# Kernel tuning notes

Measured on AMD Instinct MI355X. Metric: run time of the kernel, lower is better.

Reference implementation:

```python
import jax, jax.numpy as jnp
import numpy as np

N, D = 8192, 4096  # D must be a power of 2 for FWHT


def fwht(x):
    """Unnormalized Fast Walsh-Hadamard Transform along the last axis (len = 2^k)."""
    orig_shape = x.shape
    d = orig_shape[-1]
    x = x.reshape(-1, d)
    h = 1
    while h < d:
        x = x.reshape(-1, d // (2 * h), 2, h)
        a = x[..., 0, :]
        b = x[..., 1, :]
        x = jnp.stack([a + b, a - b], axis=-2)
        h *= 2
    return x.reshape(orig_shape)


def setup_inputs() -> dict:
    key = jax.random.key(0)
    k = jax.random.split(key, 6)
    return {
        "x": jax.random.normal(k[0], (N, D), dtype=jnp.float32),
        "s1": jax.random.normal(k[1], (D,), dtype=jnp.float32),
        "s2": jax.random.normal(k[2], (D,), dtype=jnp.float32),
        "g_mu": jax.random.normal(k[3], (D,), dtype=jnp.float32),
        "g_rho": jax.random.normal(k[4], (D,), dtype=jnpp.float32) if False else jax.random.normal(k[4], (D,), dtype=jnp.float32),
        "epsilon": jax.random.normal(k[5], (D,), dtype=jnp.float32),
    }


def reference(x, s1, s2, g_mu, g_rho, epsilon):
    # W(u) = diag(s1) H diag(u) H diag(s2); forward (sample=True):
    #   b = x @ W(g_mu).T + x @ W(softplus(g_rho) * epsilon).T
    # Per-row (H symmetric): x @ W(u).T = s1 * fwht(u * fwht(s2 * x)).
    t = fwht(x * s2)                                  # [N, D], shared between both terms
    g_noise = jax.nn.softplus(g_rho) * epsilon        # g_sigma_sqrt @ epsilon
    b = s1 * fwht(t * g_mu) + s1 * fwht(t * g_noise)  # [N, D]
    return b
```

## Files before the change

### kernel.cpp

```cpp
#include <hip/hip_runtime.h>
#include <math.h>

#define D 4096

__device__ __forceinline__ void fwht64(float* v) {
#pragma unroll
    for (int h = 1; h < 64; h <<= 1) {
#pragma unroll
        for (int i = 0; i < 64; i += 2 * h) {
#pragma unroll
            for (int j = i; j < i + h; ++j) {
                const float a = v[j];
                const float b = v[j + h];
                v[j]     = a + b;
                v[j + h] = a - b;
            }
        }
    }
}

__global__ void whvi_prep(const float* __restrict__ g_mu,
                          const float* __restrict__ g_rho,
                          const float* __restrict__ eps,
                          float* __restrict__ gq) {
    const int i = blockIdx.x * 64 + threadIdx.x;
    const int l = i >> 6, k = i & 63;
    const int e = (l & 3) | (k << 2) | ((l >> 2) << 8);
    const float r  = g_rho[e];
    const float sp = (r > 20.f) ? r : log1pf(expf(r));
    gq[i] = g_mu[e] + sp * eps[e];
}

__global__ void __launch_bounds__(64) whvi_main(
    const float* __restrict__ x,  const float* __restrict__ s1,
    const float* __restrict__ s2, const float* __restrict__ gq,
    const float* __restrict__ g_mu, const float* __restrict__ g_rho,
    const float* __restrict__ eps, float* __restrict__ out) {
    __shared__ alignas(16) float lds[D];
    const int l = threadIdx.x;
    const long long row = blockIdx.x;
    const float* xr = x + row * (long long)D;
    float v[64];

#pragma unroll
    for (int q = 0; q < 16; ++q) {
        const int base = (l << 2) + (q << 8);
        const float4 xv = *reinterpret_cast<const float4*>(xr + base);
        const float4 sv = *reinterpret_cast<const float4*>(s2 + base);
        v[4 * q + 0] = xv.x * sv.x;
        v[4 * q + 1] = xv.y * sv.y;
        v[4 * q + 2] = xv.z * sv.z;
        v[4 * q + 3] = xv.w * sv.w;
    }

    fwht64(v);

#pragma unroll
    for (int q = 0; q < 16; ++q) {
        const int addr = ((l ^ (q & 7)) << 2) + (q << 8);
        *reinterpret_cast<float4*>(&lds[addr]) =
            make_float4(v[4 * q], v[4 * q + 1], v[4 * q + 2], v[4 * q + 3]);
    }
    __syncthreads();
    {
        const int xb = (l & 3) | ((l >> 2) << 8);
        const int mk = (l >> 2) & 7;
#pragma unroll
        for (int k = 0; k < 64; ++k)
            v[k] = lds[xb + ((k ^ mk) << 2)];
    }

    fwht64(v);

    if (gq) {
#pragma unroll
        for (int m = 0; m < 16; ++m) {
            const float4 gv = *reinterpret_cast<const float4*>(gq + l * 64 + 4 * m);
            v[4 * m + 0] *= gv.x;
            v[4 * m + 1] *= gv.y;
            v[4 * m + 2] *= gv.z;
            v[4 * m + 3] *= gv.w;
        }
    } else {
#pragma unroll
        for (int k = 0; k < 64; ++k) {
            const int e = (l & 3) | (k << 2) | ((l >> 2) << 8);
            const float r  = g_rho[e];
            const float sp = (r > 20.f) ? r : log1pf(expf(r));
            v[k] *= g_mu[e] + sp * eps[e];
        }
    }

    fwht64(v);

    __syncthreads();
    {
        const int xb = (l & 3) | ((l >> 2) << 8);
        const int mk = (l >> 2) & 7;
#pragma unroll
        for (int k = 0; k < 64; ++k)
            lds[xb + ((k ^ mk) << 2)] = v[k];
    }
    __syncthreads();
#pragma unroll
    for (int q = 0; q < 16; ++q) {
        const int addr = ((l ^ (q & 7)) << 2) + (q << 8);
        const float4 t = *reinterpret_cast<const float4*>(&lds[addr]);
        v[4 * q + 0] = t.x;
        v[4 * q + 1] = t.y;
        v[4 * q + 2] = t.z;
        v[4 * q + 3] = t.w;
    }

    fwht64(v);

    float* outr = out + row * (long long)D;
#pragma unroll
    for (int q = 0; q < 16; ++q) {
        const int base = (l << 2) + (q << 8);
        const float4 sv = *reinterpret_cast<const float4*>(s1 + base);
        float4 o;
        o.x = v[4 * q + 0] * sv.x;
        o.y = v[4 * q + 1] * sv.y;
        o.z = v[4 * q + 2] * sv.z;
        o.w = v[4 * q + 3] * sv.w;
        *reinterpret_cast<float4*>(outr + base) = o;
    }
}

extern "C" void kernel_launch(void* const* d_in, const int* in_sizes, int n_in,
                              void* d_out, int out_size, void* d_ws, size_t ws_size,
                              hipStream_t stream) {
    const float* x     = (const float*)d_in[0];
    const float* s1    = (const float*)d_in[1];
    const float* s2    = (const float*)d_in[2];
    const float* g_mu  = (const float*)d_in[3];
    const float* g_rho = (const float*)d_in[4];
    const float* eps   = (const float*)d_in[5];
    float* out = (float*)d_out;
    const int rows = in_sizes[0] / D;

    float* gq = nullptr;
    if (ws_size >= (size_t)D * sizeof(float)) {
        gq = (float*)d_ws;
        whvi_prep<<<D / 64, 64, 0, stream>>>(g_mu, g_rho, eps, gq);
    }
    whvi_main<<<rows, 64, 0, stream>>>(x, s1, s2, gq, g_mu, g_rho, eps, out);
}
```

Before: 249.9 us.

## Halve LDS footprint by doing each transpose in two half-passes

The shared-memory transpose between FWHT stages now uses a 2048-float buffer instead of 4096. Each transpose runs as two sequential half-exchanges: each half-wave writes its half, reads its half, then swaps roles, with extra barriers in between. A min-blocks hint of 4 is added to the launch bounds. The goal is to fit more single-wave blocks per CU to hide global-memory latency, at the cost of extra barriers and LDS round trips.

```diff
diff --git a/kernel.cpp b/kernel.cpp
--- a/kernel.cpp
+++ b/kernel.cpp
@@ -31,16 +31,20 @@
     gq[i] = g_mu[e] + sp * eps[e];
 }
 
-__global__ void __launch_bounds__(64) whvi_main(
+__global__ void __launch_bounds__(64, 4) whvi_main(
     const float* __restrict__ x,  const float* __restrict__ s1,
     const float* __restrict__ s2, const float* __restrict__ gq,
     const float* __restrict__ g_mu, const float* __restrict__ g_rho,
     const float* __restrict__ eps, float* __restrict__ out) {
-    __shared__ alignas(16) float lds[D];
-    const int l = threadIdx.x;
+    __shared__ alignas(16) float lds[2048];
+    const int l  = threadIdx.x;
+    const int hi = l >> 5;
     const long long row = blockIdx.x;
     const float* xr = x + row * (long long)D;
     float v[64];
+
+#define WA(q) ((((l ^ ((q) & 7)) & 31) << 2) + ((q) << 7))
+#define RB(k) (xb + ((((k) ^ mk) & 31) << 2))
 
 #pragma unroll
     for (int q = 0; q < 16; ++q) {
@@ -55,19 +59,47 @@
 
     fwht64(v);
 
-#pragma unroll
-    for (int q = 0; q < 16; ++q) {
-        const int addr = ((l ^ (q & 7)) << 2) + (q << 8);
-        *reinterpret_cast<float4*>(&lds[addr]) =
-            make_float4(v[4 * q], v[4 * q + 1], v[4 * q + 2], v[4 * q + 3]);
-    }
-    __syncthreads();
-    {
-        const int xb = (l & 3) | ((l >> 2) << 8);
-        const int mk = (l >> 2) & 7;
-#pragma unroll
-        for (int k = 0; k < 64; ++k)
-            v[k] = lds[xb + ((k ^ mk) << 2)];
+    const int mk = (l >> 2) & 7;
+    const int xb = (l & 3) + ((l >> 2) << 7);
+
+    if (hi == 0) {
+#pragma unroll
+        for (int q = 0; q < 8; ++q)
+            *reinterpret_cast<float4*>(&lds[WA(q)]) =
+                make_float4(v[4*q], v[4*q+1], v[4*q+2], v[4*q+3]);
+    } else {
+#pragma unroll
+        for (int q = 8; q < 16; ++q)
+            *reinterpret_cast<float4*>(&lds[WA(q)]) =
+                make_float4(v[4*q], v[4*q+1], v[4*q+2], v[4*q+3]);
+    }
+    __syncthreads();
+    if (hi == 0) {
+#pragma unroll
+        for (int k = 0; k < 32; ++k) v[k] = lds[RB(k)];
+    } else {
+#pragma unroll
+        for (int k = 32; k < 64; ++k) v[k] = lds[RB(k)];
+    }
+    __syncthreads();
+    if (hi == 0) {
+#pragma unroll
+        for (int q = 8; q < 16; ++q)
+            *reinterpret_cast<float4*>(&lds[WA(q)]) =
+                make_float4(v[4*q], v[4*q+1], v[4*q+2], v[4*q+3]);
+    } else {
+#pragma unroll
+        for (int q = 0; q < 8; ++q)
+            *reinterpret_cast<float4*>(&lds[WA(q)]) =
+                make_float4(v[4*q], v[4*q+1], v[4*q+2], v[4*q+3]);
+    }
+    __syncthreads();
+    if (hi == 0) {
+#pragma unroll
+        for (int k = 32; k < 64; ++k) v[k] = lds[RB(k)];
+    } else {
+#pragma unroll
+        for (int k = 0; k < 32; ++k) v[k] = lds[RB(k)];
     }
 
     fwht64(v);
@@ -94,22 +126,48 @@
     fwht64(v);
 
     __syncthreads();
-    {
-        const int xb = (l & 3) | ((l >> 2) << 8);
-        const int mk = (l >> 2) & 7;
-#pragma unroll
-        for (int k = 0; k < 64; ++k)
-            lds[xb + ((k ^ mk) << 2)] = v[k];
-    }
-    __syncthreads();
-#pragma unroll
-    for (int q = 0; q < 16; ++q) {
-        const int addr = ((l ^ (q & 7)) << 2) + (q << 8);
-        const float4 t = *reinterpret_cast<const float4*>(&lds[addr]);
-        v[4 * q + 0] = t.x;
-        v[4 * q + 1] = t.y;
-        v[4 * q + 2] = t.z;
-        v[4 * q + 3] = t.w;
+    if (hi == 0) {
+#pragma unroll
+        for (int k = 0; k < 32; ++k) lds[RB(k)] = v[k];
+    } else {
+#pragma unroll
+        for (int k = 32; k < 64; ++k) lds[RB(k)] = v[k];
+    }
+    __syncthreads();
+    if (hi == 0) {
+#pragma unroll
+        for (int q = 0; q < 8; ++q) {
+            const float4 t = *reinterpret_cast<const float4*>(&lds[WA(q)]);
+            v[4*q+0] = t.x; v[4*q+1] = t.y; v[4*q+2] = t.z; v[4*q+3] = t.w;
+        }
+    } else {
+#pragma unroll
+        for (int q = 8; q < 16; ++q) {
+            const float4 t = *reinterpret_cast<const float4*>(&lds[WA(q)]);
+            v[4*q+0] = t.x; v[4*q+1] = t.y; v[4*q+2] = t.z; v[4*q+3] = t.w;
+        }
+    }
+    __syncthreads();
+    if (hi == 0) {
+#pragma unroll
+        for (int k = 32; k < 64; ++k) lds[RB(k)] = v[k];
+    } else {
+#pragma unroll
+        for (int k = 0; k < 32; ++k) lds[RB(k)] = v[k];
+    }
+    __syncthreads();
+    if (hi == 0) {
+#pragma unroll
+        for (int q = 8; q < 16; ++q) {
+            const float4 t = *reinterpret_cast<const float4*>(&lds[WA(q)]);
+            v[4*q+0] = t.x; v[4*q+1] = t.y; v[4*q+2] = t.z; v[4*q+3] = t.w;
+        }
+    } else {
+#pragma unroll
+        for (int q = 0; q < 8; ++q) {
+            const float4 t = *reinterpret_cast<const float4*>(&lds[WA(q)]);
+            v[4*q+0] = t.x; v[4*q+1] = t.y; v[4*q+2] = t.z; v[4*q+3] = t.w;
+        }
     }
 
     fwht64(v);
@@ -126,6 +184,8 @@
         o.w = v[4 * q + 3] * sv.w;
         *reinterpret_cast<float4*>(outr + base) = o;
     }
+#undef WA
+#undef RB
 }
 
 extern "C" void kernel_launch(void* const* d_in, const int* in_sizes, int n_in,
```

After: 475.2 us. 1.9x slower.
